# Kernel optimization log

Measured on AMD Instinct MI355X. Metric: run time of the kernel, lower is better.

Reference implementation:

```python
import jax, jax.numpy as jnp
import numpy as np
import math

B, N, D = 8, 515, 1024
H, DH, L = 8, 64, 4
FF = 4 * D            # SwiGLU inner dim
ROT = 32              # rotary dim = min(32, dim_head)
NB, MAXD = 32, 128    # rel-pos buckets / max distance
SCALE = 16.0          # cosine_sim_scale
EPS = 1e-5


def layer_norm(x, g, stable=False, eps=EPS):
    if stable:
        x = x / jax.lax.stop_gradient(jnp.max(x, axis=-1, keepdims=True))
    m = jnp.mean(x, axis=-1, keepdims=True)
    v = jnp.mean(jnp.square(x - m), axis=-1, keepdims=True)  # biased var
    return (x - m) * jax.lax.rsqrt(v + eps) * g


def l2norm(t):
    return t / jnp.linalg.norm(t, axis=-1, keepdims=True)


def rotary_cos_sin(n):
    inv_freq = 1.0 / (10000.0 ** (jnp.arange(0, ROT, 2, dtype=jnp.float32) / ROT))
    freqs = jnp.arange(n, dtype=jnp.float32)[:, None] * inv_freq[None, :]  # [n, ROT/2]
    freqs = jnp.repeat(freqs, 2, axis=-1)                                   # [n, ROT]
    return jnp.cos(freqs), jnp.sin(freqs)


def rotate_half(t):  # interleaved pairs: (x0,x1) -> (-x1,x0)
    t1, t2 = t[..., 0::2], t[..., 1::2]
    return jnp.stack((-t2, t1), axis=-1).reshape(t.shape)


def apply_rot(t, cos, sin):
    t_rot, t_pass = t[..., :ROT], t[..., ROT:]
    t_rot = t_rot * cos + rotate_half(t_rot) * sin
    return jnp.concatenate([t_rot, t_pass], axis=-1)


def rel_pos_bias(i, j, emb):
    q_pos = jnp.arange(i)
    k_pos = jnp.arange(j)
    rel = k_pos[None, :] - q_pos[:, None]  # [i, j]
    n = jnp.maximum(-rel, 0)
    max_exact = NB // 2
    is_small = n < max_exact
    nf = jnp.maximum(n, 1).astype(jnp.float32)
    val_large = max_exact + (jnp.log(nf / max_exact) / math.log(MAXD / max_exact) * (NB - max_exact)).astype(jnp.int32)
    val_large = jnp.minimum(val_large, NB - 1)
    bucket = jnp.where(is_small, n, val_large)
    return jnp.transpose(emb[bucket], (2, 0, 1))  # [H, i, j]


def _forward(x, attn_norm_g, Wq, Wkv, bkv, null_kv, Wo, out_norm_g,
             ff_norm_g, Wff1, Wff2, relpos_emb, final_norm_g, Wproj):
    b, n = x.shape[0], x.shape[1]
    bias = rel_pos_bias(n, n + 1, relpos_emb)      # [H, n, n+1]
    cos, sin = rotary_cos_sin(n)
    neg = -jnp.finfo(x.dtype).max
    causal = jnp.arange(n + 1)[None, :] >= jnp.arange(n)[:, None] + 2  # triu(2) on [n, n+1]
    for l in range(L):
        xn = layer_norm(x, attn_norm_g[l])
        q = (xn @ Wq[l]).reshape(b, n, H, DH).transpose(0, 2, 1, 3) * SCALE  # [b,h,n,dh]
        kv = xn @ Wkv[l] + bkv[l]                                            # [b,n,2dh]
        k, v = kv[..., :DH], kv[..., DH:]
        q = apply_rot(q, cos, sin)
        k = apply_rot(k, cos, sin)
        nk = jnp.broadcast_to(null_kv[l, 0], (b, 1, DH))
        nv = jnp.broadcast_to(null_kv[l, 1], (b, 1, DH))
        k = jnp.concatenate([nk, k], axis=1)  # [b, n+1, dh]
        v = jnp.concatenate([nv, v], axis=1)
        q = l2norm(q) * math.sqrt(SCALE)
        k = l2norm(k) * math.sqrt(SCALE)
        sim = jnp.einsum('bhid,bjd->bhij', q, k) + bias[None]
        sim = jnp.where(causal[None, None], neg, sim)
        attn = jax.nn.softmax(sim.astype(jnp.float32), axis=-1).astype(sim.dtype)
        o = jnp.einsum('bhij,bjd->bhid', attn, v)
        o = o.transpose(0, 2, 1, 3).reshape(b, n, H * DH)
        x = x + layer_norm(o @ Wo[l], out_norm_g[l])
        h = layer_norm(x, ff_norm_g[l]) @ Wff1[l]   # [b,n,2*FF]
        a, g = h[..., :FF], h[..., FF:]
        x = x + (a * jax.nn.silu(g)) @ Wff2[l]
    return layer_norm(x, final_norm_g, stable=True) @ Wproj


def setup_inputs() -> dict:
    key = jax.random.key(0)
    ks = jax.random.split(key, 10)
    def nrm(k, shape, scale=1.0):
        return jax.random.normal(k, shape, jnp.float32) * scale
    return {
        'x': nrm(ks[0], (B, N, D)),
        'attn_norm_g': jnp.ones((L, D), jnp.float32),
        'Wq': nrm(ks[1], (L, D, H * DH), D ** -0.5),
        'Wkv': nrm(ks[2], (L, D, 2 * DH), D ** -0.5),
        'bkv': jnp.zeros((L, 2 * DH), jnp.float32),
        'null_kv': nrm(ks[3], (L, 2, DH)),
        'Wo': nrm(ks[4], (L, H * DH, D), (H * DH) ** -0.5),
        'out_norm_g': jnp.ones((L, D), jnp.float32),
        'ff_norm_g': jnp.ones((L, D), jnp.float32),
        'Wff1': nrm(ks[5], (L, D, 2 * FF), D ** -0.5),
        'Wff2': nrm(ks[6], (L, FF, D), FF ** -0.5),
        'relpos_emb': nrm(ks[7], (NB, H), 0.02),
        'final_norm_g': jnp.ones((D,), jnp.float32),
        'Wproj': nrm(ks[8], (D, D), D ** -0.5),
    }


def reference(x, attn_norm_g, Wq, Wkv, bkv, null_kv, Wo, out_norm_g,
              ff_norm_g, Wff1, Wff2, relpos_emb, final_norm_g, Wproj):
    return _forward(x, attn_norm_g, Wq, Wkv, bkv, null_kv, Wo, out_norm_g,
                    ff_norm_g, Wff1, Wff2, relpos_emb, final_norm_g, Wproj)
```

## Files before the change

### kernel.cpp

```cpp
#include <hip/hip_runtime.h>
#include <cmath>

namespace {

constexpr int kB = 8, kN = 515, kD = 1024, kH = 8, kDH = 64, kL = 4;
constexpr int kFF = 4096, kROT = 32;
constexpr int kNK = kN + 1;
constexpr int kNKP = 576;
constexpr int kM = kB * kN;
constexpr float kEPS = 1e-5f;

typedef _Float16 half_t;
typedef _Float16 half8 __attribute__((ext_vector_type(8)));
typedef float f32x4 __attribute__((ext_vector_type(4)));

__device__ __forceinline__ float wave_sum(float v) {
#pragma unroll
    for (int o = 32; o > 0; o >>= 1) v += __shfl_xor(v, o);
    return v;
}
__device__ __forceinline__ float wave_max(float v) {
#pragma unroll
    for (int o = 32; o > 0; o >>= 1) v = fmaxf(v, __shfl_xor(v, o));
    return v;
}

template<int MODE>
__global__ void ln_kernel(const float* __restrict__ in, const float* __restrict__ g,
                          float* __restrict__ out) {
    int row = blockIdx.x;
    const float4* inr = (const float4*)(in + (size_t)row * kD);
    float4 v = inr[threadIdx.x];
    __shared__ float red[4];
    int lane = threadIdx.x & 63, wid = threadIdx.x >> 6;

    if (MODE == 2) {
        float mx = fmaxf(fmaxf(v.x, v.y), fmaxf(v.z, v.w));
        mx = wave_max(mx);
        if (lane == 0) red[wid] = mx;
        __syncthreads();
        mx = fmaxf(fmaxf(red[0], red[1]), fmaxf(red[2], red[3]));
        __syncthreads();
        float inv = 1.0f / mx;
        v.x *= inv; v.y *= inv; v.z *= inv; v.w *= inv;
    }

    float s = v.x + v.y + v.z + v.w;
    s = wave_sum(s);
    if (lane == 0) red[wid] = s;
    __syncthreads();
    float mean = (red[0] + red[1] + red[2] + red[3]) * (1.0f / kD);
    __syncthreads();

    float dx = v.x - mean, dy = v.y - mean, dz = v.z - mean, dw = v.w - mean;
    float ss = dx * dx + dy * dy + dz * dz + dw * dw;
    ss = wave_sum(ss);
    if (lane == 0) red[wid] = ss;
    __syncthreads();
    float var = (red[0] + red[1] + red[2] + red[3]) * (1.0f / kD);
    float r = 1.0f / sqrtf(var + kEPS);

    float4 g4 = ((const float4*)g)[threadIdx.x];
    float4 o4 = make_float4(dx * r * g4.x, dy * r * g4.y, dz * r * g4.z, dw * r * g4.w);
    float4* op = (float4*)(out + (size_t)row * kD);
    if (MODE == 1) {
        float4 c = op[threadIdx.x];
        o4.x += c.x; o4.y += c.y; o4.z += c.z; o4.w += c.w;
    }
    op[threadIdx.x] = o4;
}

template<int ILV>
__global__ void tcvt_kernel(const float* __restrict__ src, half_t* __restrict__ dst,
                            int K, int N, int pitch, int rowOff) {
    __shared__ float tile[32][33];
    int tx = threadIdx.x & 31, ty = threadIdx.x >> 5;
    int n0 = blockIdx.x * 32, k0 = blockIdx.y * 32;
#pragma unroll
    for (int j = 0; j < 4; ++j)
        tile[ty + 8 * j][tx] = src[(size_t)(k0 + ty + 8 * j) * N + n0 + tx];
    __syncthreads();
#pragma unroll
    for (int j = 0; j < 4; ++j) {
        int n = n0 + ty + 8 * j;
        int rowp;
        if (ILV == 0) {
            rowp = rowOff + n;
        } else {
            if (n < kFF) rowp = ((n >> 4) << 5) + (n & 15);
            else { int c = n - kFF; rowp = ((c >> 4) << 5) + 16 + (c & 15); }
        }
        dst[(size_t)rowp * pitch + k0 + tx] = (half_t)tile[tx][ty + 8 * j];
    }
}

template<int AF16, int EPI>
__global__ __launch_bounds__(256)
void mm_kernel(const float* __restrict__ Af, const half_t* __restrict__ Ah,
               const half_t* __restrict__ Bt,
               float* __restrict__ Cf, half_t* __restrict__ Ch,
               float* __restrict__ C2, const float* __restrict__ bias,
               int Mm, int Nn, int Kk) {
    constexpr int PADK = 40;
    __shared__ half_t As[128 * PADK];
    __shared__ half_t Bs[128 * PADK];
    const int m0 = blockIdx.y * 128, n0 = blockIdx.x * 128;
    const int t = threadIdx.x, lane = t & 63, wid = t >> 6;
    const int wr = wid >> 1, wc = wid & 1;
    const int srow = t >> 1, skh = (t & 1) * 16;

    f32x4 acc[4][4] = {};

    const int arow = m0 + srow;
    const bool aval = arow < Mm;
    const float*  aptr  = Af + (size_t)arow * Kk + skh;
    const half_t* ahptr = Ah + (size_t)arow * Kk + skh;
    const half_t* bptr  = Bt + (size_t)(n0 + srow) * Kk + skh;
    half_t* asl = &As[srow * PADK + skh];
    half_t* bsl = &Bs[srow * PADK + skh];

    const int kg = (lane >> 4) * 8;
    const int rl = lane & 15;

    for (int k0 = 0; k0 < Kk; k0 += 32) {
        half8 h0 = {0, 0, 0, 0, 0, 0, 0, 0}, h1 = {0, 0, 0, 0, 0, 0, 0, 0};
        if (AF16) {
            if (aval) { h0 = *(const half8*)ahptr; h1 = *(const half8*)(ahptr + 8); }
            ahptr += 32;
        } else {
            if (aval) {
                const float4* a4 = (const float4*)aptr;
                float4 f0 = a4[0], f1 = a4[1], f2 = a4[2], f3 = a4[3];
                h0 = half8{(half_t)f0.x, (half_t)f0.y, (half_t)f0.z, (half_t)f0.w,
                           (half_t)f1.x, (half_t)f1.y, (half_t)f1.z, (half_t)f1.w};
                h1 = half8{(half_t)f2.x, (half_t)f2.y, (half_t)f2.z, (half_t)f2.w,
                           (half_t)f3.x, (half_t)f3.y, (half_t)f3.z, (half_t)f3.w};
            }
            aptr += 32;
        }
        *(half8*)asl = h0;
        *(half8*)(asl + 8) = h1;
        *(half8*)bsl = *(const half8*)bptr;
        *(half8*)(bsl + 8) = *(const half8*)(bptr + 8);
        bptr += 32;
        __syncthreads();

        half8 af[4], bf[4];
#pragma unroll
        for (int i = 0; i < 4; ++i)
            af[i] = *(const half8*)&As[(wr * 64 + i * 16 + rl) * PADK + kg];
#pragma unroll
        for (int j = 0; j < 4; ++j)
            bf[j] = *(const half8*)&Bs[(wc * 64 + j * 16 + rl) * PADK + kg];
#pragma unroll
        for (int i = 0; i < 4; ++i)
#pragma unroll
            for (int j = 0; j < 4; ++j)
                acc[i][j] = __builtin_amdgcn_mfma_f32_16x16x32_f16(af[i], bf[j], acc[i][j], 0, 0, 0);
        __syncthreads();
    }

#pragma unroll
    for (int i = 0; i < 4; ++i) {
        int rbase = m0 + wr * 64 + i * 16 + (lane >> 4) * 4;
#pragma unroll
        for (int r = 0; r < 4; ++r) {
            int row = rbase + r;
            if (row >= Mm) continue;
            if (EPI == 4) {
#pragma unroll
                for (int j = 0; j < 4; j += 2) {
                    int ccbase = n0 + wc * 64 + j * 16;
                    int col = (ccbase >> 5) * 16 + rl;
                    float a = acc[i][j][r];
                    float g = acc[i][j + 1][r];
                    float sg = g / (1.0f + expf(-g));
                    Ch[(size_t)row * (Nn >> 1) + col] = (half_t)(a * sg);
                }
            } else {
#pragma unroll
                for (int j = 0; j < 4; ++j) {
                    int col = n0 + wc * 64 + j * 16 + rl;
                    float vvv = acc[i][j][r];
                    if (EPI == 0) {
                        Cf[(size_t)row * Nn + col] = vvv;
                    } else if (EPI == 1) {
                        if (col < 512) Cf[(size_t)row * 512 + col] = vvv;
                        else C2[(size_t)row * 128 + (col - 512)] = vvv + bias[col - 512];
                    } else if (EPI == 2) {
                        Cf[(size_t)row * Nn + col] += vvv;
                    } else {
                        Ch[(size_t)row * Nn + col] = (half_t)vvv;
                    }
                }
            }
        }
    }
}

__global__ void qrot_kernel(const float* __restrict__ q, half_t* __restrict__ Qh) {
    int row = blockIdx.x * 4 + (threadIdx.x >> 6);
    int lane = threadIdx.x & 63;
    int h = row % kH;
    int bn = row / kH;
    int b = bn / kN, n = bn % kN;
    float t = q[(size_t)row * kDH + lane];
    float partner = __shfl_xor(t, 1);
    if (lane < kROT) {
        float e = (float)(lane & ~1) / (float)kROT;
        float inv = powf(10000.0f, -e);
        float ang = (float)n * inv;
        float c = cosf(ang), s = sinf(ang);
        t = (lane & 1) ? fmaf(t, c, partner * s) : fmaf(t, c, -partner * s);
    }
    float ss = wave_sum(t * t);
    float sc = 4.0f / sqrtf(ss);
    Qh[(((size_t)b * kH + h) * kNKP + n) * kDH + lane] = (half_t)(t * sc);
}

__global__ void krot_kernel(const float* __restrict__ kv, const float* __restrict__ nullkv,
                            half_t* __restrict__ Kh, half_t* __restrict__ VTh) {
    int row = blockIdx.x * 4 + (threadIdx.x >> 6);
    int lane = threadIdx.x & 63;
    int b = row / kNKP, jj = row % kNKP;
    float tk = 0.f, tv = 0.f;
    if (jj == 0) {
        tk = nullkv[lane];
        tv = nullkv[64 + lane];
    } else if (jj < kNK) {
        size_t base = ((size_t)(b * kN + jj - 1)) * 128;
        tk = kv[base + lane];
        tv = kv[base + 64 + lane];
    }
    float partner = __shfl_xor(tk, 1);
    if (jj != 0 && jj < kNK && lane < kROT) {
        float e = (float)(lane & ~1) / (float)kROT;
        float inv = powf(10000.0f, -e);
        float ang = (float)(jj - 1) * inv;
        float c = cosf(ang), s = sinf(ang);
        tk = (lane & 1) ? fmaf(tk, c, partner * s) : fmaf(tk, c, -partner * s);
    }
    float ss = wave_sum(tk * tk);
    float sc = (jj < kNK) ? 4.0f / sqrtf(ss) : 0.f;
    Kh[(size_t)row * kDH + lane] = (half_t)(tk * sc);
    VTh[((size_t)b * kDH + lane) * kNKP + jj] = (half_t)tv;
}

__global__ void dbias_kernel(const float* __restrict__ emb, float* __restrict__ db) {
    int t = blockIdx.x * 256 + threadIdx.x;
    if (t >= kH * 516) return;
    int h = t / 516, idx = t % 516;
    int nn = idx - 1; if (nn < 0) nn = 0;
    int bucket;
    if (nn < 16) bucket = nn;
    else {
        float lf = logf((float)nn * (1.0f / 16.0f));
        int vl = 16 + (int)(lf / logf(8.0f) * 16.0f);
        bucket = vl < 31 ? vl : 31;
    }
    db[t] = emb[bucket * kH + h];
}

__global__ __launch_bounds__(256)
void fattn_kernel(const half_t* __restrict__ Qh, const half_t* __restrict__ Kh,
                  const half_t* __restrict__ VTh, const float* __restrict__ dbias,
                  float* __restrict__ o) {
    const int qt = blockIdx.x, h = blockIdx.y, b = blockIdx.z;
    const int t = threadIdx.x, lane = t & 63, w = t >> 6;
    const int rl = lane & 15, g = lane >> 4;
    const int q0 = qt * 64, qw0 = q0 + w * 16;

    __shared__ half_t Ps[4][16][72];
    __shared__ float db[520];
    for (int i = t; i < 516; i += 256) db[i] = dbias[h * 516 + i];
    __syncthreads();

    const half_t* qbase = Qh + (((size_t)b * kH + h) * kNKP + qw0 + rl) * kDH;
    half8 qa0 = *(const half8*)(qbase + g * 8);
    half8 qa1 = *(const half8*)(qbase + 32 + g * 8);

    float m[4] = {-1e30f, -1e30f, -1e30f, -1e30f};
    float l[4] = {0.f, 0.f, 0.f, 0.f};
    f32x4 Oa[4] = {};

    const int wktiles = min((qw0 + 16) / 64 + 1, kNKP / 64);

    for (int kt = 0; kt < wktiles; ++kt) {
        const int jt = kt * 64;
        f32x4 sc[4];
#pragma unroll
        for (int f = 0; f < 4; ++f) {
            const half_t* kp = Kh + ((size_t)b * kNKP + jt + f * 16 + rl) * kDH + g * 8;
            half8 kb0 = *(const half8*)kp;
            half8 kb1 = *(const half8*)(kp + 32);
            f32x4 a = {};
            a = __builtin_amdgcn_mfma_f32_16x16x32_f16(qa0, kb0, a, 0, 0, 0);
            a = __builtin_amdgcn_mfma_f32_16x16x32_f16(qa1, kb1, a, 0, 0, 0);
            sc[f] = a;
        }
        float tm[4] = {-1e30f, -1e30f, -1e30f, -1e30f};
#pragma unroll
        for (int f = 0; f < 4; ++f) {
            int jb = jt + f * 16 + rl;
#pragma unroll
            for (int r = 0; r < 4; ++r) {
                int qq = qw0 + 4 * g + r;
                int idx = qq - jb + 1;
                int ic = idx < 0 ? 0 : (idx > 515 ? 515 : idx);
                float s = sc[f][r] + db[ic];
                s = (idx < 0) ? -1e30f : s;
                sc[f][r] = s;
                tm[r] = fmaxf(tm[r], s);
            }
        }
#pragma unroll
        for (int off = 1; off < 16; off <<= 1)
#pragma unroll
            for (int r = 0; r < 4; ++r) tm[r] = fmaxf(tm[r], __shfl_xor(tm[r], off));
        float scal[4], tsum[4];
#pragma unroll
        for (int r = 0; r < 4; ++r) {
            float nm = fmaxf(m[r], tm[r]);
            scal[r] = __expf(m[r] - nm);
            m[r] = nm;
            tsum[r] = 0.f;
        }
#pragma unroll
        for (int f = 0; f < 4; ++f)
#pragma unroll
            for (int r = 0; r < 4; ++r) {
                float p = __expf(sc[f][r] - m[r]);
                tsum[r] += p;
                Ps[w][4 * g + r][f * 16 + rl] = (half_t)p;
            }
#pragma unroll
        for (int r = 0; r < 4; ++r) l[r] = l[r] * scal[r] + tsum[r];
#pragma unroll
        for (int fd = 0; fd < 4; ++fd)
#pragma unroll
            for (int r = 0; r < 4; ++r) Oa[fd][r] *= scal[r];
        half8 pa0 = *(const half8*)&Ps[w][rl][g * 8];
        half8 pa1 = *(const half8*)&Ps[w][rl][32 + g * 8];
#pragma unroll
        for (int fd = 0; fd < 4; ++fd) {
            const half_t* vp = VTh + ((size_t)b * kDH + fd * 16 + rl) * kNKP + jt + g * 8;
            half8 vb0 = *(const half8*)vp;
            half8 vb1 = *(const half8*)(vp + 32);
            Oa[fd] = __builtin_amdgcn_mfma_f32_16x16x32_f16(pa0, vb0, Oa[fd], 0, 0, 0);
            Oa[fd] = __builtin_amdgcn_mfma_f32_16x16x32_f16(pa1, vb1, Oa[fd], 0, 0, 0);
        }
    }

    float inv[4];
#pragma unroll
    for (int r = 0; r < 4; ++r) {
        float L = l[r];
#pragma unroll
        for (int off = 1; off < 16; off <<= 1) L += __shfl_xor(L, off);
        inv[r] = 1.0f / L;
    }
#pragma unroll
    for (int fd = 0; fd < 4; ++fd)
#pragma unroll
        for (int r = 0; r < 4; ++r) {
            int qq = qw0 + 4 * g + r;
            if (qq < kN)
                o[((size_t)(b * kN + qq) * kH + h) * kDH + fd * 16 + rl] = Oa[fd][r] * inv[r];
        }
}

}

extern "C" void kernel_launch(void* const* d_in, const int* in_sizes, int n_in,
                              void* d_out, int out_size, void* d_ws, size_t ws_size,
                              hipStream_t stream) {
    const float* x_in   = (const float*)d_in[0];
    const float* attn_g = (const float*)d_in[1];
    const float* Wq     = (const float*)d_in[2];
    const float* Wkv    = (const float*)d_in[3];
    const float* bkv    = (const float*)d_in[4];
    const float* nullkv = (const float*)d_in[5];
    const float* Wo     = (const float*)d_in[6];
    const float* out_g  = (const float*)d_in[7];
    const float* ff_g   = (const float*)d_in[8];
    const float* Wff1   = (const float*)d_in[9];
    const float* Wff2   = (const float*)d_in[10];
    const float* emb    = (const float*)d_in[11];
    const float* fin_g  = (const float*)d_in[12];
    const float* Wproj  = (const float*)d_in[13];
    float* out = (float*)d_out;

    char* wsb = (char*)d_ws;
    size_t off = 0;
    auto alloc = [&](size_t bytes) -> void* {
        void* p = wsb + off;
        off += (bytes + 255) & ~(size_t)255;
        return p;
    };
    float*  bx    = (float*)alloc((size_t)kM * kD * 4);
    float*  bxn   = (float*)alloc((size_t)kM * kD * 4);
    float*  bt    = (float*)alloc((size_t)kM * kD * 4);
    float*  bq    = (float*)alloc((size_t)kM * 512 * 4);
    float*  bo    = (float*)alloc((size_t)kM * 512 * 4);
    float*  bkvb  = (float*)alloc((size_t)kM * 128 * 4);
    half_t* Qh    = (half_t*)alloc((size_t)kB * kH * kNKP * kDH * 2);
    half_t* Kh    = (half_t*)alloc((size_t)kB * kNKP * kDH * 2);
    half_t* VTh   = (half_t*)alloc((size_t)kB * kDH * kNKP * 2);
    float*  dbias = (float*)alloc((size_t)kH * 516 * 4);
    half_t* bg    = (half_t*)alloc((size_t)kM * kFF * 2);
    half_t* WqkvT = (half_t*)alloc((size_t)640 * kD * 2);
    half_t* WoT   = (half_t*)alloc((size_t)kD * 512 * 2);
    half_t* Wff1T = (half_t*)alloc((size_t)2 * kFF * kD * 2);
    half_t* Wff2T = (half_t*)alloc((size_t)kD * kFF * 2);

    hipMemcpyAsync(bx, x_in, (size_t)kM * kD * 4, hipMemcpyDeviceToDevice, stream);
    dbias_kernel<<<(kH * 516 + 255) / 256, 256, 0, stream>>>(emb, dbias);

    const int mt = (kM + 127) / 128;

    for (int l = 0; l < kL; ++l) {
        tcvt_kernel<0><<<dim3(512 / 32, kD / 32), 256, 0, stream>>>(
            Wq + (size_t)l * kD * 512, WqkvT, kD, 512, kD, 0);
        tcvt_kernel<0><<<dim3(128 / 32, kD / 32), 256, 0, stream>>>(
            Wkv + (size_t)l * kD * 128, WqkvT, kD, 128, kD, 512);
        tcvt_kernel<0><<<dim3(kD / 32, 512 / 32), 256, 0, stream>>>(
            Wo + (size_t)l * 512 * kD, WoT, 512, kD, 512, 0);
        tcvt_kernel<1><<<dim3(2 * kFF / 32, kD / 32), 256, 0, stream>>>(
            Wff1 + (size_t)l * kD * 2 * kFF, Wff1T, kD, 2 * kFF, kD, 0);
        tcvt_kernel<0><<<dim3(kD / 32, kFF / 32), 256, 0, stream>>>(
            Wff2 + (size_t)l * kFF * kD, Wff2T, kFF, kD, kFF, 0);

        ln_kernel<0><<<kM, 256, 0, stream>>>(bx, attn_g + (size_t)l * kD, bxn);
        mm_kernel<0, 1><<<dim3(640 / 128, mt), 256, 0, stream>>>(
            bxn, nullptr, WqkvT, bq, nullptr, bkvb, bkv + (size_t)l * 128, kM, 640, kD);
        qrot_kernel<<<kM * kH / 4, 256, 0, stream>>>(bq, Qh);
        krot_kernel<<<kB * kNKP / 4, 256, 0, stream>>>(bkvb, nullkv + (size_t)l * 128, Kh, VTh);
        fattn_kernel<<<dim3(kNKP / 64, kH, kB), 256, 0, stream>>>(Qh, Kh, VTh, dbias, bo);
        mm_kernel<0, 0><<<dim3(kD / 128, mt), 256, 0, stream>>>(
            bo, nullptr, WoT, bt, nullptr, nullptr, nullptr, kM, kD, 512);
        ln_kernel<1><<<kM, 256, 0, stream>>>(bt, out_g + (size_t)l * kD, bx);
        ln_kernel<0><<<kM, 256, 0, stream>>>(bx, ff_g + (size_t)l * kD, bxn);
        mm_kernel<0, 4><<<dim3(2 * kFF / 128, mt), 256, 0, stream>>>(
            bxn, nullptr, Wff1T, nullptr, bg, nullptr, nullptr, kM, 2 * kFF, kD);
        mm_kernel<1, 2><<<dim3(kD / 128, mt), 256, 0, stream>>>(
            nullptr, bg, Wff2T, bx, nullptr, nullptr, nullptr, kM, kD, kFF);
    }

    ln_kernel<2><<<kM, 256, 0, stream>>>(bx, fin_g, bxn);
    tcvt_kernel<0><<<dim3(kD / 32, kD / 32), 256, 0, stream>>>(Wproj, (half_t*)Wff1T, kD, kD, kD, 0);
    mm_kernel<0, 0><<<dim3(kD / 128, mt), 256, 0, stream>>>(
        bxn, nullptr, (half_t*)Wff1T, out, nullptr, nullptr, nullptr, kM, kD, kD);
}
```

Before: 1.997 ms.

## Feed GEMMs fp16 activations via direct global-to-LDS loads and fuse LN pair

LayerNorm and attention outputs are now written as fp16, so every GEMM reads half-precision A operands. The GEMM loads tiles with global_load_lds straight into unpadded LDS, skipping the register staging and in-kernel float-to-half conversion. The post-attention LayerNorm, residual add and the pre-FF LayerNorm are fused into one kernel, saving a pass over the activations. The unpadded LDS layout may cause bank conflicts on fragment reads, and the single-buffered loop still waits at the barrier on each load.

```diff
diff --git a/kernel.cpp b/kernel.cpp
--- a/kernel.cpp
+++ b/kernel.cpp
@@ -12,6 +12,7 @@
 
 typedef _Float16 half_t;
 typedef _Float16 half8 __attribute__((ext_vector_type(8)));
+typedef _Float16 half4 __attribute__((ext_vector_type(4)));
 typedef float f32x4 __attribute__((ext_vector_type(4)));
 
 __device__ __forceinline__ float wave_sum(float v) {
@@ -25,12 +26,17 @@
     return v;
 }
 
+__device__ __forceinline__ void gload_lds16(const half_t* g, half_t* l) {
+    __builtin_amdgcn_global_load_lds(
+        (const __attribute__((address_space(1))) void*)g,
+        (__attribute__((address_space(3))) void*)l, 16, 0, 0);
+}
+
 template<int MODE>
 __global__ void ln_kernel(const float* __restrict__ in, const float* __restrict__ g,
-                          float* __restrict__ out) {
+                          half_t* __restrict__ out) {
     int row = blockIdx.x;
-    const float4* inr = (const float4*)(in + (size_t)row * kD);
-    float4 v = inr[threadIdx.x];
+    float4 v = ((const float4*)(in + (size_t)row * kD))[threadIdx.x];
     __shared__ float red[4];
     int lane = threadIdx.x & 63, wid = threadIdx.x >> 6;
 
@@ -61,13 +67,58 @@
     float r = 1.0f / sqrtf(var + kEPS);
 
     float4 g4 = ((const float4*)g)[threadIdx.x];
-    float4 o4 = make_float4(dx * r * g4.x, dy * r * g4.y, dz * r * g4.z, dw * r * g4.w);
-    float4* op = (float4*)(out + (size_t)row * kD);
-    if (MODE == 1) {
-        float4 c = op[threadIdx.x];
-        o4.x += c.x; o4.y += c.y; o4.z += c.z; o4.w += c.w;
-    }
-    op[threadIdx.x] = o4;
+    half4 o4 = {(half_t)(dx * r * g4.x), (half_t)(dy * r * g4.y),
+                (half_t)(dz * r * g4.z), (half_t)(dw * r * g4.w)};
+    ((half4*)(out + (size_t)row * kD))[threadIdx.x] = o4;
+}
+
+__global__ void ln_add_ln_kernel(const float* __restrict__ in, const float* __restrict__ g1,
+                                 float* __restrict__ res, const float* __restrict__ g2,
+                                 half_t* __restrict__ outh) {
+    int row = blockIdx.x;
+    float4 v = ((const float4*)(in + (size_t)row * kD))[threadIdx.x];
+    __shared__ float red[4];
+    int lane = threadIdx.x & 63, wid = threadIdx.x >> 6;
+
+    float s = v.x + v.y + v.z + v.w;
+    s = wave_sum(s);
+    if (lane == 0) red[wid] = s;
+    __syncthreads();
+    float mean = (red[0] + red[1] + red[2] + red[3]) * (1.0f / kD);
+    __syncthreads();
+    float dx = v.x - mean, dy = v.y - mean, dz = v.z - mean, dw = v.w - mean;
+    float ss = dx * dx + dy * dy + dz * dz + dw * dw;
+    ss = wave_sum(ss);
+    if (lane == 0) red[wid] = ss;
+    __syncthreads();
+    float var = (red[0] + red[1] + red[2] + red[3]) * (1.0f / kD);
+    float r = 1.0f / sqrtf(var + kEPS);
+
+    float4 g4 = ((const float4*)g1)[threadIdx.x];
+    float4 res4 = ((const float4*)(res + (size_t)row * kD))[threadIdx.x];
+    float4 nv = make_float4(res4.x + dx * r * g4.x, res4.y + dy * r * g4.y,
+                            res4.z + dz * r * g4.z, res4.w + dw * r * g4.w);
+    ((float4*)(res + (size_t)row * kD))[threadIdx.x] = nv;
+    __syncthreads();
+
+    float s2 = nv.x + nv.y + nv.z + nv.w;
+    s2 = wave_sum(s2);
+    if (lane == 0) red[wid] = s2;
+    __syncthreads();
+    float mean2 = (red[0] + red[1] + red[2] + red[3]) * (1.0f / kD);
+    __syncthreads();
+    float ex = nv.x - mean2, ey = nv.y - mean2, ez = nv.z - mean2, ew = nv.w - mean2;
+    float ss2 = ex * ex + ey * ey + ez * ez + ew * ew;
+    ss2 = wave_sum(ss2);
+    if (lane == 0) red[wid] = ss2;
+    __syncthreads();
+    float var2 = (red[0] + red[1] + red[2] + red[3]) * (1.0f / kD);
+    float r2 = 1.0f / sqrtf(var2 + kEPS);
+
+    float4 h4 = ((const float4*)g2)[threadIdx.x];
+    half4 o4 = {(half_t)(ex * r2 * h4.x), (half_t)(ey * r2 * h4.y),
+                (half_t)(ez * r2 * h4.z), (half_t)(ew * r2 * h4.w)};
+    ((half4*)(outh + (size_t)row * kD))[threadIdx.x] = o4;
 }
 
 template<int ILV>
@@ -94,64 +145,49 @@
     }
 }
 
-template<int AF16, int EPI>
+template<int EPI>
 __global__ __launch_bounds__(256)
-void mm_kernel(const float* __restrict__ Af, const half_t* __restrict__ Ah,
-               const half_t* __restrict__ Bt,
+void mm_kernel(const half_t* __restrict__ A, const half_t* __restrict__ Bt,
                float* __restrict__ Cf, half_t* __restrict__ Ch,
                float* __restrict__ C2, const float* __restrict__ bias,
                int Mm, int Nn, int Kk) {
-    constexpr int PADK = 40;
-    __shared__ half_t As[128 * PADK];
-    __shared__ half_t Bs[128 * PADK];
+    __shared__ half_t As[128 * 32];
+    __shared__ half_t Bs[128 * 32];
     const int m0 = blockIdx.y * 128, n0 = blockIdx.x * 128;
-    const int t = threadIdx.x, lane = t & 63, wid = t >> 6;
-    const int wr = wid >> 1, wc = wid & 1;
-    const int srow = t >> 1, skh = (t & 1) * 16;
+    const int t = threadIdx.x, lane = t & 63, w = t >> 6;
+    const int wr = w >> 1, wc = w & 1;
+    const int rl = lane & 15, g = lane >> 4;
+
+    const int srow = w * 32 + (lane >> 2);
+    const int scol = (lane & 3) * 8;
+    int ar0 = m0 + srow;        ar0 = ar0 < Mm ? ar0 : Mm - 1;
+    int ar1 = m0 + srow + 16;   ar1 = ar1 < Mm ? ar1 : Mm - 1;
+    const half_t* ag0 = A + (size_t)ar0 * Kk + scol;
+    const half_t* ag1 = A + (size_t)ar1 * Kk + scol;
+    const half_t* bg0 = Bt + (size_t)(n0 + srow) * Kk + scol;
+    const half_t* bg1 = Bt + (size_t)(n0 + srow + 16) * Kk + scol;
+    half_t* asl0 = As + (w * 32) * 32;
+    half_t* asl1 = As + (w * 32 + 16) * 32;
+    half_t* bsl0 = Bs + (w * 32) * 32;
+    half_t* bsl1 = Bs + (w * 32 + 16) * 32;
 
     f32x4 acc[4][4] = {};
 
-    const int arow = m0 + srow;
-    const bool aval = arow < Mm;
-    const float*  aptr  = Af + (size_t)arow * Kk + skh;
-    const half_t* ahptr = Ah + (size_t)arow * Kk + skh;
-    const half_t* bptr  = Bt + (size_t)(n0 + srow) * Kk + skh;
-    half_t* asl = &As[srow * PADK + skh];
-    half_t* bsl = &Bs[srow * PADK + skh];
-
-    const int kg = (lane >> 4) * 8;
-    const int rl = lane & 15;
-
     for (int k0 = 0; k0 < Kk; k0 += 32) {
-        half8 h0 = {0, 0, 0, 0, 0, 0, 0, 0}, h1 = {0, 0, 0, 0, 0, 0, 0, 0};
-        if (AF16) {
-            if (aval) { h0 = *(const half8*)ahptr; h1 = *(const half8*)(ahptr + 8); }
-            ahptr += 32;
-        } else {
-            if (aval) {
-                const float4* a4 = (const float4*)aptr;
-                float4 f0 = a4[0], f1 = a4[1], f2 = a4[2], f3 = a4[3];
-                h0 = half8{(half_t)f0.x, (half_t)f0.y, (half_t)f0.z, (half_t)f0.w,
-                           (half_t)f1.x, (half_t)f1.y, (half_t)f1.z, (half_t)f1.w};
-                h1 = half8{(half_t)f2.x, (half_t)f2.y, (half_t)f2.z, (half_t)f2.w,
-                           (half_t)f3.x, (half_t)f3.y, (half_t)f3.z, (half_t)f3.w};
-            }
-            aptr += 32;
-        }
-        *(half8*)asl = h0;
-        *(half8*)(asl + 8) = h1;
-        *(half8*)bsl = *(const half8*)bptr;
-        *(half8*)(bsl + 8) = *(const half8*)(bptr + 8);
-        bptr += 32;
+        gload_lds16(ag0, asl0);
+        gload_lds16(ag1, asl1);
+        gload_lds16(bg0, bsl0);
+        gload_lds16(bg1, bsl1);
+        ag0 += 32; ag1 += 32; bg0 += 32; bg1 += 32;
         __syncthreads();
 
         half8 af[4], bf[4];
 #pragma unroll
         for (int i = 0; i < 4; ++i)
-            af[i] = *(const half8*)&As[(wr * 64 + i * 16 + rl) * PADK + kg];
+            af[i] = *(const half8*)&As[(wr * 64 + i * 16 + rl) * 32 + g * 8];
 #pragma unroll
         for (int j = 0; j < 4; ++j)
-            bf[j] = *(const half8*)&Bs[(wc * 64 + j * 16 + rl) * PADK + kg];
+            bf[j] = *(const half8*)&Bs[(wc * 64 + j * 16 + rl) * 32 + g * 8];
 #pragma unroll
         for (int i = 0; i < 4; ++i)
 #pragma unroll
@@ -162,7 +198,7 @@
 
 #pragma unroll
     for (int i = 0; i < 4; ++i) {
-        int rbase = m0 + wr * 64 + i * 16 + (lane >> 4) * 4;
+        int rbase = m0 + wr * 64 + i * 16 + g * 4;
 #pragma unroll
         for (int r = 0; r < 4; ++r) {
             int row = rbase + r;
@@ -173,8 +209,8 @@
                     int ccbase = n0 + wc * 64 + j * 16;
                     int col = (ccbase >> 5) * 16 + rl;
                     float a = acc[i][j][r];
-                    float g = acc[i][j + 1][r];
-                    float sg = g / (1.0f + expf(-g));
+                    float gv = acc[i][j + 1][r];
+                    float sg = gv / (1.0f + expf(-gv));
                     Ch[(size_t)row * (Nn >> 1) + col] = (half_t)(a * sg);
                 }
             } else {
@@ -189,8 +225,6 @@
                         else C2[(size_t)row * 128 + (col - 512)] = vvv + bias[col - 512];
                     } else if (EPI == 2) {
                         Cf[(size_t)row * Nn + col] += vvv;
-                    } else {
-                        Ch[(size_t)row * Nn + col] = (half_t)vvv;
                     }
                 }
             }
@@ -264,7 +298,7 @@
 __global__ __launch_bounds__(256)
 void fattn_kernel(const half_t* __restrict__ Qh, const half_t* __restrict__ Kh,
                   const half_t* __restrict__ VTh, const float* __restrict__ dbias,
-                  float* __restrict__ o) {
+                  half_t* __restrict__ o) {
     const int qt = blockIdx.x, h = blockIdx.y, b = blockIdx.z;
     const int t = threadIdx.x, lane = t & 63, w = t >> 6;
     const int rl = lane & 15, g = lane >> 4;
@@ -365,7 +399,8 @@
         for (int r = 0; r < 4; ++r) {
             int qq = qw0 + 4 * g + r;
             if (qq < kN)
-                o[((size_t)(b * kN + qq) * kH + h) * kDH + fd * 16 + rl] = Oa[fd][r] * inv[r];
+                o[((size_t)(b * kN + qq) * kH + h) * kDH + fd * 16 + rl] =
+                    (half_t)(Oa[fd][r] * inv[r]);
         }
 }
 
@@ -398,10 +433,10 @@
         return p;
     };
     float*  bx    = (float*)alloc((size_t)kM * kD * 4);
-    float*  bxn   = (float*)alloc((size_t)kM * kD * 4);
     float*  bt    = (float*)alloc((size_t)kM * kD * 4);
+    half_t* bxn   = (half_t*)alloc((size_t)kM * kD * 2);
     float*  bq    = (float*)alloc((size_t)kM * 512 * 4);
-    float*  bo    = (float*)alloc((size_t)kM * 512 * 4);
+    half_t* bo    = (half_t*)alloc((size_t)kM * 512 * 2);
     float*  bkvb  = (float*)alloc((size_t)kM * 128 * 4);
     half_t* Qh    = (half_t*)alloc((size_t)kB * kH * kNKP * kDH * 2);
     half_t* Kh    = (half_t*)alloc((size_t)kB * kNKP * kDH * 2);
@@ -431,23 +466,23 @@
             Wff2 + (size_t)l * kFF * kD, Wff2T, kFF, kD, kFF, 0);
 
         ln_kernel<0><<<kM, 256, 0, stream>>>(bx, attn_g + (size_t)l * kD, bxn);
-        mm_kernel<0, 1><<<dim3(640 / 128, mt), 256, 0, stream>>>(
-            bxn, nullptr, WqkvT, bq, nullptr, bkvb, bkv + (size_t)l * 128, kM, 640, kD);
+        mm_kernel<1><<<dim3(640 / 128, mt), 256, 0, stream>>>(
+            bxn, WqkvT, bq, nullptr, bkvb, bkv + (size_t)l * 128, kM, 640, kD);
         qrot_kernel<<<kM * kH / 4, 256, 0, stream>>>(bq, Qh);
         krot_kernel<<<kB * kNKP / 4, 256, 0, stream>>>(bkvb, nullkv + (size_t)l * 128, Kh, VTh);
         fattn_kernel<<<dim3(kNKP / 64, kH, kB), 256, 0, stream>>>(Qh, Kh, VTh, dbias, bo);
-        mm_kernel<0, 0><<<dim3(kD / 128, mt), 256, 0, stream>>>(
-            bo, nullptr, WoT, bt, nullptr, nullptr, nullptr, kM, kD, 512);
-        ln_kernel<1><<<kM, 256, 0, stream>>>(bt, out_g + (size_t)l * kD, bx);
-        ln_kernel<0><<<kM, 256, 0, stream>>>(bx, ff_g + (size_t)l * kD, bxn);
-        mm_kernel<0, 4><<<dim3(2 * kFF / 128, mt), 256, 0, stream>>>(
-            bxn, nullptr, Wff1T, nullptr, bg, nullptr, nullptr, kM, 2 * kFF, kD);
-        mm_kernel<1, 2><<<dim3(kD / 128, mt), 256, 0, stream>>>(
-            nullptr, bg, Wff2T, bx, nullptr, nullptr, nullptr, kM, kD, kFF);
+        mm_kernel<0><<<dim3(kD / 128, mt), 256, 0, stream>>>(
+            bo, WoT, bt, nullptr, nullptr, nullptr, kM, kD, 512);
+        ln_add_ln_kernel<<<kM, 256, 0, stream>>>(
+            bt, out_g + (size_t)l * kD, bx, ff_g + (size_t)l * kD, bxn);
+        mm_kernel<4><<<dim3(2 * kFF / 128, mt), 256, 0, stream>>>(
+            bxn, Wff1T, nullptr, bg, nullptr, nullptr, kM, 2 * kFF, kD);
+        mm_kernel<2><<<dim3(kD / 128, mt), 256, 0, stream>>>(
+            bg, Wff2T, bx, nullptr, nullptr, nullptr, kM, kD, kFF);
     }
 
     ln_kernel<2><<<kM, 256, 0, stream>>>(bx, fin_g, bxn);
     tcvt_kernel<0><<<dim3(kD / 32, kD / 32), 256, 0, stream>>>(Wproj, (half_t*)Wff1T, kD, kD, kD, 0);
-    mm_kernel<0, 0><<<dim3(kD / 128, mt), 256, 0, stream>>>(
-        bxn, nullptr, (half_t*)Wff1T, out, nullptr, nullptr, nullptr, kM, kD, kD);
-}
+    mm_kernel<0><<<dim3(kD / 128, mt), 256, 0, stream>>>(
+        bxn, (half_t*)Wff1T, out, nullptr, nullptr, nullptr, kM, kD, kD);
+}
```

Result: faster. 1.745 ms (-12.6%).
